# Optimization experiments

Hardware: AMD Instinct MI355X
Metric: run time of the kernel (lower is better)

Reference implementation:

```python
import jax, jax.numpy as jnp
import numpy as np

N, E, D = 100000, 1600000, 128      # nodes, edges, in_channels = MLP out_dim
L = 3                               # num GIN layers
OC = D + L * D                      # concat width = 512
CH, CHID = 4, 256                   # num ChannelMLPs, their hidden dim


def setup_inputs() -> dict:
    key = jax.random.key(0)
    ks = jax.random.split(key, 10)
    s = lambda fan_in: 1.0 / np.sqrt(fan_in)
    x = jax.random.normal(ks[0], (N, D), dtype=jnp.float32)
    edge_index = jax.random.randint(ks[1], (2, E), 0, N, dtype=jnp.int32)
    # conv MLPs: per layer 3 linear layers (in->hid, hid->hid, hid->out), all 128x128
    convW = jax.random.normal(ks[2], (L, 3, D, D), dtype=jnp.float32) * s(D)
    convB = jnp.zeros((L, 3, D), dtype=jnp.float32)
    # channel MLPs: 512 -> 256 -> 256 -> 1, ReLU after every layer (output_activation='relu')
    chanW1 = jax.random.normal(ks[3], (CH, OC, CHID), dtype=jnp.float32) * s(OC)
    chanB1 = jnp.zeros((CH, CHID), dtype=jnp.float32)
    chanW2 = jax.random.normal(ks[4], (CH, CHID, CHID), dtype=jnp.float32) * s(CHID)
    chanB2 = jnp.zeros((CH, CHID), dtype=jnp.float32)
    chanW3 = jax.random.normal(ks[5], (CH, CHID, 1), dtype=jnp.float32) * s(CHID)
    chanB3 = jnp.zeros((CH, 1), dtype=jnp.float32)
    return {"x": x, "edge_index": edge_index, "convW": convW, "convB": convB,
            "chanW1": chanW1, "chanB1": chanB1, "chanW2": chanW2, "chanB2": chanB2,
            "chanW3": chanW3, "chanB3": chanB3}


def reference(x, edge_index, convW, convB, chanW1, chanB1, chanW2, chanB2, chanW3, chanB3):
    src, dst = edge_index[0], edge_index[1]
    n = x.shape[0]
    feats = [x]                      # skip_first_features=False -> keep input
    h = x
    for l in range(L):
        # GINConv, eps=0: mlp((1+eps)*h + sum_{j in N(i)} h_j)
        agg = jax.ops.segment_sum(h[src], dst, num_segments=n)  # scatter-add at targets
        h = h + agg
        for k in range(3):           # MLP: Lin+ReLU x3 (2 hidden + relu output activation)
            h = jax.nn.relu(h @ convW[l, k] + convB[l, k])
        feats.append(h)
    xcat = jnp.concatenate(feats, axis=1)                       # [N, 512]
    # channel MLPs vectorized over the channel axis c
    h1 = jax.nn.relu(jnp.einsum('nd,cdh->cnh', xcat, chanW1) + chanB1[:, None, :])
    h2 = jax.nn.relu(jnp.einsum('cnh,chk->cnk', h1, chanW2) + chanB2[:, None, :])
    h3 = jax.nn.relu(jnp.einsum('cnh,cho->cno', h2, chanW3) + chanB3[:, None, :])
    return jnp.transpose(h3[..., 0])                            # [N, num_ChannelMLPs]
```

## Files before the change

### kernel.cpp

```cpp
#include <hip/hip_runtime.h>
#include <hip/hip_bf16.h>

#define D 128
#define NLAYER 3
#define NCH 4

typedef __attribute__((ext_vector_type(8))) short short8;
typedef __attribute__((ext_vector_type(4))) float f32x4;

__device__ __forceinline__ ushort f2bf(float f) {
    unsigned int u = __builtin_bit_cast(unsigned int, f);
    u += 0x7fffu + ((u >> 16) & 1u);
    return (ushort)(u >> 16);
}
__device__ __forceinline__ float bflo(unsigned int u) {
    return __builtin_bit_cast(float, u << 16);
}
__device__ __forceinline__ float bfhi(unsigned int u) {
    return __builtin_bit_cast(float, u & 0xffff0000u);
}

#define FILL_CHUNK 4096
__global__ __launch_bounds__(256) void hist_part_kernel(
    const int* __restrict__ dst, int* __restrict__ deg,
    int E, int nPer, int N)
{
    int cls = blockIdx.x & 7;
    int base = (blockIdx.x >> 3) * FILL_CHUNK;
    int lo = cls * nPer;
    int hi = lo + nPer; if (hi > N) hi = N;
    int end = base + FILL_CHUNK; if (end > E) end = E;
    for (int e = base + threadIdx.x; e < end; e += 256) {
        int d = dst[e];
        if (d >= lo && d < hi) atomicAdd(&deg[d], 1);
    }
}

__global__ __launch_bounds__(256) void blocksum_kernel(
    const int* __restrict__ deg, int* __restrict__ bsum, int n)
{
    int i = blockIdx.x * 256 + threadIdx.x;
    int v = (i < n) ? deg[i] : 0;
#pragma unroll
    for (int o = 1; o < 64; o <<= 1) v += __shfl_xor(v, o);
    __shared__ int s[4];
    if ((threadIdx.x & 63) == 0) s[threadIdx.x >> 6] = v;
    __syncthreads();
    if (threadIdx.x == 0) bsum[blockIdx.x] = s[0] + s[1] + s[2] + s[3];
}

__global__ __launch_bounds__(512) void scanblk_kernel(
    const int* __restrict__ bsum, int* __restrict__ boff, int nb,
    int* __restrict__ offs, int n, int E)
{
    __shared__ int sh[512];
    int t = threadIdx.x;
    sh[t] = (t < nb) ? bsum[t] : 0;
    __syncthreads();
    for (int d = 1; d < 512; d <<= 1) {
        int v = (t >= d) ? sh[t - d] : 0;
        __syncthreads();
        sh[t] += v;
        __syncthreads();
    }
    if (t < nb) boff[t] = (t == 0) ? 0 : sh[t - 1];
    if (t == 0) offs[n] = E;
}

__global__ __launch_bounds__(256) void blockscan_kernel(
    const int* __restrict__ deg, const int* __restrict__ boff,
    int* __restrict__ offs, int* __restrict__ cursor, int n)
{
    __shared__ int sh[256];
    int t = threadIdx.x;
    int i = blockIdx.x * 256 + t;
    int v = (i < n) ? deg[i] : 0;
    sh[t] = v;
    __syncthreads();
    for (int d = 1; d < 256; d <<= 1) {
        int u = (t >= d) ? sh[t - d] : 0;
        __syncthreads();
        sh[t] += u;
        __syncthreads();
    }
    if (i < n) {
        int ex = boff[blockIdx.x] + sh[t] - v;
        offs[i] = ex; cursor[i] = ex;
    }
}

__global__ __launch_bounds__(256) void fill_part_kernel(
    const int* __restrict__ src, const int* __restrict__ dst,
    int* __restrict__ cursor, int* __restrict__ csr,
    int E, int nPer, int N)
{
    int cls = blockIdx.x & 7;
    int base = (blockIdx.x >> 3) * FILL_CHUNK;
    int lo = cls * nPer;
    int hi = lo + nPer; if (hi > N) hi = N;
    int end = base + FILL_CHUNK; if (end > E) end = E;
    for (int e = base + threadIdx.x; e < end; e += 256) {
        int d = dst[e];
        int s = src[e];
        if (d >= lo && d < hi) {
            int p = atomicAdd(&cursor[d], 1);
            csr[p] = s;
        }
    }
}

__global__ __launch_bounds__(256) void cvtx_kernel(
    const float* __restrict__ x, ushort* __restrict__ xb, int total8)
{
    int i = blockIdx.x * 256 + threadIdx.x;
    if (i >= total8) return;
    const float* gp = x + (size_t)i * 8;
    float4 v0 = *(const float4*)gp;
    float4 v1 = *(const float4*)(gp + 4);
    short8 pk;
    pk[0] = (short)f2bf(v0.x); pk[1] = (short)f2bf(v0.y);
    pk[2] = (short)f2bf(v0.z); pk[3] = (short)f2bf(v0.w);
    pk[4] = (short)f2bf(v1.x); pk[5] = (short)f2bf(v1.y);
    pk[6] = (short)f2bf(v1.z); pk[7] = (short)f2bf(v1.w);
    *(short8*)(xb + (size_t)i * 8) = pk;
}

__global__ void cvtW_kernel(const float* __restrict__ W, ushort* __restrict__ Wt,
                            int K, int Ncols) {
    __shared__ float tile[32][33];
    int c = blockIdx.z;
    int k0 = blockIdx.x * 32, n0 = blockIdx.y * 32;
    const float* Wc = W + (size_t)c * K * Ncols;
    ushort* Wtc = Wt + (size_t)c * K * Ncols;
    int tx = threadIdx.x & 31, ty = threadIdx.x >> 5;
#pragma unroll
    for (int i = 0; i < 4; ++i) {
        int k = k0 + ty + i * 8;
        tile[ty + i * 8][tx] = Wc[(size_t)k * Ncols + n0 + tx];
    }
    __syncthreads();
#pragma unroll
    for (int i = 0; i < 4; ++i) {
        int n = n0 + ty + i * 8;
        Wtc[(size_t)n * K + k0 + tx] = f2bf(tile[tx][ty + i * 8]);
    }
}

__global__ __launch_bounds__(256) void agg_bf16(
    const ushort* __restrict__ h,
    const int* __restrict__ offs, const int* __restrict__ csr,
    ushort* __restrict__ outb, int n)
{
    int node = (blockIdx.x * 256 + threadIdx.x) >> 4;
    int l16 = threadIdx.x & 15;
    if (node >= n) return;
    uint4 u = *((const uint4*)(h + (size_t)node * 128) + l16);
    float a0 = bflo(u.x), a1 = bfhi(u.x);
    float a2 = bflo(u.y), a3 = bfhi(u.y);
    float a4 = bflo(u.z), a5 = bfhi(u.z);
    float a6 = bflo(u.w), a7 = bfhi(u.w);
    int b = offs[node], e = offs[node + 1];
    int j = b;
    for (; j + 4 <= e; j += 4) {
        int s0 = csr[j], s1 = csr[j + 1], s2 = csr[j + 2], s3 = csr[j + 3];
        uint4 v0 = *((const uint4*)(h + (size_t)s0 * 128) + l16);
        uint4 v1 = *((const uint4*)(h + (size_t)s1 * 128) + l16);
        uint4 v2 = *((const uint4*)(h + (size_t)s2 * 128) + l16);
        uint4 v3 = *((const uint4*)(h + (size_t)s3 * 128) + l16);
        a0 += (bflo(v0.x) + bflo(v1.x)) + (bflo(v2.x) + bflo(v3.x));
        a1 += (bfhi(v0.x) + bfhi(v1.x)) + (bfhi(v2.x) + bfhi(v3.x));
        a2 += (bflo(v0.y) + bflo(v1.y)) + (bflo(v2.y) + bflo(v3.y));
        a3 += (bfhi(v0.y) + bfhi(v1.y)) + (bfhi(v2.y) + bfhi(v3.y));
        a4 += (bflo(v0.z) + bflo(v1.z)) + (bflo(v2.z) + bflo(v3.z));
        a5 += (bfhi(v0.z) + bfhi(v1.z)) + (bfhi(v2.z) + bfhi(v3.z));
        a6 += (bflo(v0.w) + bflo(v1.w)) + (bflo(v2.w) + bflo(v3.w));
        a7 += (bfhi(v0.w) + bfhi(v1.w)) + (bfhi(v2.w) + bfhi(v3.w));
    }
    for (; j < e; ++j) {
        uint4 v0 = *((const uint4*)(h + (size_t)csr[j] * 128) + l16);
        a0 += bflo(v0.x); a1 += bfhi(v0.x);
        a2 += bflo(v0.y); a3 += bfhi(v0.y);
        a4 += bflo(v0.z); a5 += bfhi(v0.z);
        a6 += bflo(v0.w); a7 += bfhi(v0.w);
    }
    uint4 po;
    po.x = (unsigned int)f2bf(a0) | ((unsigned int)f2bf(a1) << 16);
    po.y = (unsigned int)f2bf(a2) | ((unsigned int)f2bf(a3) << 16);
    po.z = (unsigned int)f2bf(a4) | ((unsigned int)f2bf(a5) << 16);
    po.w = (unsigned int)f2bf(a6) | ((unsigned int)f2bf(a7) << 16);
    *((uint4*)(outb + (size_t)node * 128) + l16) = po;
}

__global__ __launch_bounds__(256) void gin_mlp_mfma(
    const ushort* __restrict__ A,
    const ushort* __restrict__ WtL,
    const float* __restrict__ biasL,
    ushort* __restrict__ Out,
    int nrows)
{
    __shared__ __align__(16) ushort As[128 * 128];
    __shared__ __align__(16) ushort Bs[128 * 128];
    const int t = threadIdx.x;
    const int w = t >> 6, lane = t & 63;
    const int quad = lane >> 4, c15 = lane & 15;
    const int wr = w >> 1, wc = w & 1;
    const int rowbase = blockIdx.x * 128;

#pragma unroll
    for (int i = 0; i < 8; ++i) {
        int lin = (i * 4 + w) * 64 + lane;
        int row = lin >> 4, slot = lin & 15, g = slot ^ (row & 15);
        int grow = rowbase + row;
        if (grow >= nrows) grow = 0;
        const ushort* gp = A + (size_t)grow * 128 + g * 8;
        __builtin_amdgcn_global_load_lds(
            (const __attribute__((address_space(1))) void*)gp,
            (__attribute__((address_space(3))) void*)&As[(i * 4 + w) * 512],
            16, 0, 0);
    }
#pragma unroll
    for (int i = 0; i < 8; ++i) {
        int lin = (i * 4 + w) * 64 + lane;
        int n = lin >> 4, slot = lin & 15, g = slot ^ (n & 15);
        const ushort* gp = WtL + (size_t)n * 128 + g * 8;
        __builtin_amdgcn_global_load_lds(
            (const __attribute__((address_space(1))) void*)gp,
            (__attribute__((address_space(3))) void*)&Bs[(i * 4 + w) * 512],
            16, 0, 0);
    }
    __syncthreads();

    for (int s = 0; s < 3; ++s) {
        f32x4 acc[4][4];
#pragma unroll
        for (int i = 0; i < 4; ++i)
#pragma unroll
            for (int j = 0; j < 4; ++j)
#pragma unroll
                for (int r = 0; r < 4; ++r) acc[i][j][r] = 0.f;

#pragma unroll
        for (int ks = 0; ks < 4; ++ks) {
            short8 af[4], bf[4];
#pragma unroll
            for (int tr = 0; tr < 4; ++tr) {
                int r = wr * 64 + tr * 16 + c15;
                af[tr] = *(const short8*)&As[r * 128 + (((ks * 4 + quad) ^ (r & 15)) * 8)];
            }
#pragma unroll
            for (int tc = 0; tc < 4; ++tc) {
                int n = wc * 64 + tc * 16 + c15;
                bf[tc] = *(const short8*)&Bs[n * 128 + (((ks * 4 + quad) ^ (n & 15)) * 8)];
            }
#pragma unroll
            for (int tr = 0; tr < 4; ++tr)
#pragma unroll
                for (int tc = 0; tc < 4; ++tc)
                    acc[tr][tc] = __builtin_amdgcn_mfma_f32_16x16x32_bf16(
                        af[tr], bf[tc], acc[tr][tc], 0, 0, 0);
        }
        __syncthreads();

        if (s < 2) {
#pragma unroll
            for (int tc = 0; tc < 4; ++tc) {
                int col = wc * 64 + tc * 16 + c15;
                float bv = biasL[s * 128 + col];
#pragma unroll
                for (int tr = 0; tr < 4; ++tr)
#pragma unroll
                    for (int rg = 0; rg < 4; ++rg) {
                        int row = wr * 64 + tr * 16 + quad * 4 + rg;
                        As[row * 128 + (((col >> 3) ^ (row & 15)) * 8) + (col & 7)]
                            = f2bf(fmaxf(acc[tr][tc][rg] + bv, 0.f));
                    }
            }
            const ushort* Wn = WtL + (size_t)(s + 1) * 128 * 128;
#pragma unroll
            for (int i = 0; i < 8; ++i) {
                int lin = (i * 4 + w) * 64 + lane;
                int n = lin >> 4, slot = lin & 15, g = slot ^ (n & 15);
                const ushort* gp = Wn + (size_t)n * 128 + g * 8;
                __builtin_amdgcn_global_load_lds(
                    (const __attribute__((address_space(1))) void*)gp,
                    (__attribute__((address_space(3))) void*)&Bs[(i * 4 + w) * 512],
                    16, 0, 0);
            }
            __syncthreads();
        } else {
#pragma unroll
            for (int tc = 0; tc < 4; ++tc) {
                int col = wc * 64 + tc * 16 + c15;
                float bv = biasL[2 * 128 + col];
#pragma unroll
                for (int tr = 0; tr < 4; ++tr)
#pragma unroll
                    for (int rg = 0; rg < 4; ++rg) {
                        int grow = rowbase + wr * 64 + tr * 16 + quad * 4 + rg;
                        if (grow < nrows)
                            Out[(size_t)grow * 128 + col]
                                = f2bf(fmaxf(acc[tr][tc][rg] + bv, 0.f));
                    }
            }
        }
    }
}

__global__ __launch_bounds__(256, 2) void chan_fused_mfma(
    const ushort* __restrict__ A0, const ushort* __restrict__ A1,
    const ushort* __restrict__ A2, const ushort* __restrict__ A3,
    const ushort* __restrict__ Wt1,
    const float* __restrict__ b1,
    const ushort* __restrict__ Wt2,
    const float* __restrict__ b2,
    const float* __restrict__ w3,
    const float* __restrict__ b3,
    float* __restrict__ out,
    int N, int T, int chunkT)
{
    const int bid = blockIdx.x;
    const int xcd = bid & 7;
    const int idx = bid >> 3;
    const int c = idx & 3;
    const int rt = xcd * chunkT + (idx >> 2);
    if (rt >= T) return;
    const int rowbase = rt * 64;

    __shared__ __align__(16) ushort As2[2][64 * 64];
    __shared__ __align__(16) ushort Bs2[2][256 * 64];
    ushort* Ts = &Bs2[1][0];
    float (*red)[4] = (float (*)[4]) & As2[0][0];

    const int t = threadIdx.x;
    const int w = t >> 6, lane = t & 63;
    const int quad = lane >> 4, c15 = lane & 15;
    const ushort* W1c = Wt1 + (size_t)c * 256 * 512;
    const ushort* W2c = Wt2 + (size_t)c * 256 * 256;

    int a_grow[2], a_g[2];
#pragma unroll
    for (int i = 0; i < 2; ++i) {
        int lin = (i * 4 + w) * 64 + lane;
        int row = lin >> 3, slot = lin & 7;
        a_g[i] = slot ^ (row & 7);
        int g = rowbase + row;
        a_grow[i] = (g < N) ? g : 0;
    }
    auto stageA = [&](int buf, int kc) {
        int ai = kc >> 7;
        const ushort* Ab = (ai == 0) ? A0 : (ai == 1) ? A1 : (ai == 2) ? A2 : A3;
        const int within = kc & 127;
#pragma unroll
        for (int i = 0; i < 2; ++i) {
            const ushort* gp = Ab + (size_t)a_grow[i] * 128 + within + a_g[i] * 8;
            __builtin_amdgcn_global_load_lds(
                (const __attribute__((address_space(1))) void*)gp,
                (__attribute__((address_space(3))) void*)&As2[buf][(i * 4 + w) * 512],
                16, 0, 0);
        }
    };
    int b_n[8], b_g[8];
#pragma unroll
    for (int i = 0; i < 8; ++i) {
        int lin = (i * 4 + w) * 64 + lane;
        b_n[i] = lin >> 3;
        b_g[i] = (lin & 7) ^ (b_n[i] & 7);
    }
    auto stageB = [&](int buf, const ushort* Wn, int ldk, int kc) {
#pragma unroll
        for (int i = 0; i < 8; ++i) {
            const ushort* gp = Wn + (size_t)b_n[i] * ldk + kc + b_g[i] * 8;
            __builtin_amdgcn_global_load_lds(
                (const __attribute__((address_space(1))) void*)gp,
                (__attribute__((address_space(3))) void*)&Bs2[buf][(i * 4 + w) * 512],
                16, 0, 0);
        }
    };

    f32x4 acc[4][4];
#pragma unroll
    for (int i = 0; i < 4; ++i)
#pragma unroll
        for (int j = 0; j < 4; ++j)
#pragma unroll
            for (int r = 0; r < 4; ++r) acc[i][j][r] = 0.f;

    stageA(1, 0);
    stageB(1, W1c, 512, 0);
#pragma unroll
    for (int s = 0; s < 8; ++s) {
        const int cur = (s + 1) & 1;
        if (s < 7) {
            stageA(cur ^ 1, (s + 1) * 64);
            stageB(cur ^ 1, W1c, 512, (s + 1) * 64);
            asm volatile("s_waitcnt vmcnt(10)" ::: "memory");
        } else {
            asm volatile("s_waitcnt vmcnt(0)" ::: "memory");
        }
        __builtin_amdgcn_s_barrier();
        __builtin_amdgcn_sched_barrier(0);
#pragma unroll
        for (int ks = 0; ks < 2; ++ks) {
            short8 af[4], bf[4];
#pragma unroll
            for (int tr = 0; tr < 4; ++tr) {
                int r = tr * 16 + c15;
                af[tr] = *(const short8*)&As2[cur][r * 64 + (((ks * 4 + quad) ^ (r & 7)) * 8)];
            }
#pragma unroll
            for (int tc = 0; tc < 4; ++tc) {
                int n = w * 64 + tc * 16 + c15;
                bf[tc] = *(const short8*)&Bs2[cur][n * 64 + (((ks * 4 + quad) ^ (n & 7)) * 8)];
            }
#pragma unroll
            for (int tr = 0; tr < 4; ++tr)
#pragma unroll
                for (int tc = 0; tc < 4; ++tc)
                    acc[tr][tc] = __builtin_amdgcn_mfma_f32_16x16x32_bf16(
                        af[tr], bf[tc], acc[tr][tc], 0, 0, 0);
        }
        __builtin_amdgcn_s_barrier();
    }

    stageB(0, W2c, 256, 0);
#pragma unroll
    for (int tc = 0; tc < 4; ++tc) {
        int col = w * 64 + tc * 16 + c15;
        float bv = b1[c * 256 + col];
#pragma unroll
        for (int tr = 0; tr < 4; ++tr)
#pragma unroll
            for (int rg = 0; rg < 4; ++rg) {
                int row = tr * 16 + quad * 4 + rg;
                Ts[row * 256 + (((col >> 3) ^ (row & 31)) * 8) + (col & 7)]
                    = f2bf(fmaxf(acc[tr][tc][rg] + bv, 0.f));
            }
    }
    __syncthreads();

#pragma unroll
    for (int i = 0; i < 4; ++i)
#pragma unroll
        for (int j = 0; j < 4; ++j)
#pragma unroll
            for (int r = 0; r < 4; ++r) acc[i][j][r] = 0.f;

#pragma unroll
    for (int s = 0; s < 4; ++s) {
#pragma unroll
        for (int ks = 0; ks < 2; ++ks) {
            short8 af[4], bf[4];
            const int g0 = s * 8 + ks * 4 + quad;
#pragma unroll
            for (int tr = 0; tr < 4; ++tr) {
                int r = tr * 16 + c15;
                af[tr] = *(const short8*)&Ts[r * 256 + ((g0 ^ (r & 31)) * 8)];
            }
#pragma unroll
            for (int tc = 0; tc < 4; ++tc) {
                int n = w * 64 + tc * 16 + c15;
                bf[tc] = *(const short8*)&Bs2[0][n * 64 + (((ks * 4 + quad) ^ (n & 7)) * 8)];
            }
#pragma unroll
            for (int tr = 0; tr < 4; ++tr)
#pragma unroll
                for (int tc = 0; tc < 4; ++tc)
                    acc[tr][tc] = __builtin_amdgcn_mfma_f32_16x16x32_bf16(
                        af[tr], bf[tc], acc[tr][tc], 0, 0, 0);
        }
        if (s < 3) {
            __syncthreads();
            stageB(0, W2c, 256, (s + 1) * 64);
            __syncthreads();
        }
    }

    float b2v[4], w3v[4];
#pragma unroll
    for (int tc = 0; tc < 4; ++tc) {
        int col = w * 64 + tc * 16 + c15;
        b2v[tc] = b2[c * 256 + col];
        w3v[tc] = w3[c * 256 + col];
    }
    __syncthreads();
#pragma unroll
    for (int tr = 0; tr < 4; ++tr)
#pragma unroll
        for (int rg = 0; rg < 4; ++rg) {
            float p = 0.f;
#pragma unroll
            for (int tc = 0; tc < 4; ++tc)
                p += fmaxf(acc[tr][tc][rg] + b2v[tc], 0.f) * w3v[tc];
            p += __shfl_xor(p, 1);
            p += __shfl_xor(p, 2);
            p += __shfl_xor(p, 4);
            p += __shfl_xor(p, 8);
            if (c15 == 0) red[tr * 16 + quad * 4 + rg][w] = p;
        }
    __syncthreads();
    if (t < 64) {
        int grow = rowbase + t;
        if (grow < N) {
            float s = red[t][0] + red[t][1] + red[t][2] + red[t][3] + b3[c];
            out[(size_t)grow * NCH + c] = fmaxf(s, 0.f);
        }
    }
}

extern "C" void kernel_launch(void* const* d_in, const int* in_sizes, int n_in,
                              void* d_out, int out_size, void* d_ws, size_t ws_size,
                              hipStream_t stream) {
    const float* x        = (const float*)d_in[0];
    const int*   eidx     = (const int*)d_in[1];
    const float* convW    = (const float*)d_in[2];
    const float* convB    = (const float*)d_in[3];
    const float* chanW1   = (const float*)d_in[4];
    const float* chanB1   = (const float*)d_in[5];
    const float* chanW2   = (const float*)d_in[6];
    const float* chanB2   = (const float*)d_in[7];
    const float* chanW3   = (const float*)d_in[8];
    const float* chanB3   = (const float*)d_in[9];
    float* out = (float*)d_out;

    const int N = in_sizes[0] / D;
    const int E = in_sizes[1] / 2;
    const int* srcp = eidx;
    const int* dstp = eidx + E;
    const int nb = (N + 255) / 256;

    char* w = (char*)d_ws;
    auto take = [&](size_t bytes) {
        char* p = w;
        w += (bytes + 255) & ~(size_t)255;
        return p;
    };
    ushort* xb     = (ushort*)take((size_t)N * D * 2);
    ushort* h0     = (ushort*)take((size_t)N * D * 2);
    ushort* h1     = (ushort*)take((size_t)N * D * 2);
    ushort* h2     = (ushort*)take((size_t)N * D * 2);
    int*    deg    = (int*)take((size_t)N * 4);
    int*    offs   = (int*)take((size_t)(N + 1) * 4);
    int*    cursor = (int*)take((size_t)N * 4);
    int*    bsum   = (int*)take((size_t)nb * 4);
    int*    boff   = (int*)take((size_t)nb * 4);
    ushort* Wt1b   = (ushort*)take((size_t)NCH * 256 * 512 * 2);
    ushort* Wt2b   = (ushort*)take((size_t)NCH * 256 * 256 * 2);
    ushort* WtC    = (ushort*)take((size_t)NLAYER * 3 * D * D * 2);

    size_t used = (size_t)(w - (char*)d_ws);
    if (used > ws_size) return;
    size_t rem = ws_size - used;
    size_t need_gin = (((size_t)E * 4 + 255) & ~(size_t)255) + (size_t)N * D * 2;
    if (rem < need_gin) return;

    int*    csr = (int*)w;
    ushort* a   = (ushort*)(w + (((size_t)E * 4 + 255) & ~(size_t)255));

    hipMemsetAsync(deg, 0, (size_t)N * 4, stream);
    {
        int nchunks = (E + FILL_CHUNK - 1) / FILL_CHUNK;
        int nPer = (N + 7) / 8;
        hist_part_kernel<<<nchunks * 8, 256, 0, stream>>>(dstp, deg, E, nPer, N);
        blocksum_kernel<<<nb, 256, 0, stream>>>(deg, bsum, N);
        scanblk_kernel<<<1, 512, 0, stream>>>(bsum, boff, nb, offs, N, E);
        blockscan_kernel<<<nb, 256, 0, stream>>>(deg, boff, offs, cursor, N);
        fill_part_kernel<<<nchunks * 8, 256, 0, stream>>>(
            srcp, dstp, cursor, csr, E, nPer, N);
    }

    cvtx_kernel<<<(N * 16 + 255) / 256, 256, 0, stream>>>(x, xb, N * 16);
    cvtW_kernel<<<dim3(512 / 32, 256 / 32, NCH), 256, 0, stream>>>(chanW1, Wt1b, 512, 256);
    cvtW_kernel<<<dim3(256 / 32, 256 / 32, NCH), 256, 0, stream>>>(chanW2, Wt2b, 256, 256);
    cvtW_kernel<<<dim3(D / 32, D / 32, NLAYER * 3), 256, 0, stream>>>(convW, WtC, D, D);

    const int rowtiles = (N + 127) / 128;
    const int aggblocks = (N * 16 + 255) / 256;

    ushort* hbuf[NLAYER] = {h0, h1, h2};
    const ushort* prev = xb;
    for (int l = 0; l < NLAYER; ++l) {
        agg_bf16<<<aggblocks, 256, 0, stream>>>(prev, offs, csr, a, N);
        gin_mlp_mfma<<<rowtiles, 256, 0, stream>>>(
            a, WtC + (size_t)l * 3 * D * D, convB + (size_t)l * 3 * D, hbuf[l], N);
        prev = hbuf[l];
    }

    {
        const int T = (N + 63) / 64;
        const int chunkT = (T + 7) / 8;
        const int grid = 8 * chunkT * NCH;
        chan_fused_mfma<<<grid, 256, 0, stream>>>(
            xb, h0, h1, h2,
            Wt1b, chanB1, Wt2b, chanB2, chanW3, chanB3,
            out, N, T, chunkT);
    }
}
```

Measured before the change: 822.2 us.

## Load channel-MLP weight fragments directly into registers instead of LDS staging

The B-operand (weights) of both GEMMs in the fused channel MLP is now read straight from global memory into MFMA register fragments, with register double-buffering in the first GEMM. The LDS staging buffers for B are removed, so LDS use drops from about 80KB to about 48KB, and launch bounds are raised to allow 3 blocks per CU. This also removes the per-step barriers in the second GEMM. The trade-off is uncoalesced, partly exposed global/L2 loads of weights per wave, along with higher register pressure under the tighter occupancy bound.

```diff
diff --git a/kernel.cpp b/kernel.cpp
--- a/kernel.cpp
+++ b/kernel.cpp
@@ -306,7 +306,7 @@
     }
 }
 
-__global__ __launch_bounds__(256, 2) void chan_fused_mfma(
+__global__ __launch_bounds__(256, 3) void chan_fused_mfma(
     const ushort* __restrict__ A0, const ushort* __restrict__ A1,
     const ushort* __restrict__ A2, const ushort* __restrict__ A3,
     const ushort* __restrict__ Wt1,
@@ -327,8 +327,7 @@
     const int rowbase = rt * 64;
 
     __shared__ __align__(16) ushort As2[2][64 * 64];
-    __shared__ __align__(16) ushort Bs2[2][256 * 64];
-    ushort* Ts = &Bs2[1][0];
+    __shared__ __align__(16) ushort Ts[64 * 256];
     float (*red)[4] = (float (*)[4]) & As2[0][0];
 
     const int t = threadIdx.x;
@@ -359,22 +358,15 @@
                 16, 0, 0);
         }
     };
-    int b_n[8], b_g[8];
-#pragma unroll
-    for (int i = 0; i < 8; ++i) {
-        int lin = (i * 4 + w) * 64 + lane;
-        b_n[i] = lin >> 3;
-        b_g[i] = (lin & 7) ^ (b_n[i] & 7);
-    }
-    auto stageB = [&](int buf, const ushort* Wn, int ldk, int kc) {
-#pragma unroll
-        for (int i = 0; i < 8; ++i) {
-            const ushort* gp = Wn + (size_t)b_n[i] * ldk + kc + b_g[i] * 8;
-            __builtin_amdgcn_global_load_lds(
-                (const __attribute__((address_space(1))) void*)gp,
-                (__attribute__((address_space(3))) void*)&Bs2[buf][(i * 4 + w) * 512],
-                16, 0, 0);
-        }
+
+    int ncol[4];
+#pragma unroll
+    for (int tc = 0; tc < 4; ++tc) ncol[tc] = w * 64 + tc * 16 + c15;
+
+    auto loadB = [&](short8 (&dst)[4], const ushort* Wn, int ldk, int kc, int ks) {
+#pragma unroll
+        for (int tc = 0; tc < 4; ++tc)
+            dst[tc] = *(const short8*)&Wn[(size_t)ncol[tc] * ldk + kc + (ks * 4 + quad) * 8];
     };
 
     f32x4 acc[4][4];
@@ -385,47 +377,58 @@
 #pragma unroll
             for (int r = 0; r < 4; ++r) acc[i][j][r] = 0.f;
 
+    short8 bfb[2][4];
+    loadB(bfb[0], W1c, 512, 0, 0);
     stageA(1, 0);
-    stageB(1, W1c, 512, 0);
 #pragma unroll
     for (int s = 0; s < 8; ++s) {
         const int cur = (s + 1) & 1;
+        const int bb = s & 1;
+        short8 bf1[4];
+        loadB(bf1, W1c, 512, s * 64, 1);
         if (s < 7) {
+            loadB(bfb[bb ^ 1], W1c, 512, (s + 1) * 64, 0);
             stageA(cur ^ 1, (s + 1) * 64);
-            stageB(cur ^ 1, W1c, 512, (s + 1) * 64);
             asm volatile("s_waitcnt vmcnt(10)" ::: "memory");
         } else {
-            asm volatile("s_waitcnt vmcnt(0)" ::: "memory");
+            asm volatile("s_waitcnt vmcnt(4)" ::: "memory");
         }
         __builtin_amdgcn_s_barrier();
         __builtin_amdgcn_sched_barrier(0);
-#pragma unroll
-        for (int ks = 0; ks < 2; ++ks) {
-            short8 af[4], bf[4];
+        {
+            short8 af[4];
 #pragma unroll
             for (int tr = 0; tr < 4; ++tr) {
                 int r = tr * 16 + c15;
-                af[tr] = *(const short8*)&As2[cur][r * 64 + (((ks * 4 + quad) ^ (r & 7)) * 8)];
-            }
-#pragma unroll
-            for (int tc = 0; tc < 4; ++tc) {
-                int n = w * 64 + tc * 16 + c15;
-                bf[tc] = *(const short8*)&Bs2[cur][n * 64 + (((ks * 4 + quad) ^ (n & 7)) * 8)];
+                af[tr] = *(const short8*)&As2[cur][r * 64 + ((quad ^ (r & 7)) * 8)];
             }
 #pragma unroll
             for (int tr = 0; tr < 4; ++tr)
 #pragma unroll
                 for (int tc = 0; tc < 4; ++tc)
                     acc[tr][tc] = __builtin_amdgcn_mfma_f32_16x16x32_bf16(
-                        af[tr], bf[tc], acc[tr][tc], 0, 0, 0);
+                        af[tr], bfb[bb][tc], acc[tr][tc], 0, 0, 0);
+        }
+        {
+            short8 af[4];
+#pragma unroll
+            for (int tr = 0; tr < 4; ++tr) {
+                int r = tr * 16 + c15;
+                af[tr] = *(const short8*)&As2[cur][r * 64 + (((4 + quad) ^ (r & 7)) * 8)];
+            }
+#pragma unroll
+            for (int tr = 0; tr < 4; ++tr)
+#pragma unroll
+                for (int tc = 0; tc < 4; ++tc)
+                    acc[tr][tc] = __builtin_amdgcn_mfma_f32_16x16x32_bf16(
+                        af[tr], bf1[tc], acc[tr][tc], 0, 0, 0);
         }
         __builtin_amdgcn_s_barrier();
     }
 
-    stageB(0, W2c, 256, 0);
 #pragma unroll
     for (int tc = 0; tc < 4; ++tc) {
-        int col = w * 64 + tc * 16 + c15;
+        int col = ncol[tc];
         float bv = b1[c * 256 + col];
 #pragma unroll
         for (int tr = 0; tr < 4; ++tr)
@@ -451,34 +454,25 @@
         for (int ks = 0; ks < 2; ++ks) {
             short8 af[4], bf[4];
             const int g0 = s * 8 + ks * 4 + quad;
+            loadB(bf, W2c, 256, s * 64, ks);
 #pragma unroll
             for (int tr = 0; tr < 4; ++tr) {
                 int r = tr * 16 + c15;
                 af[tr] = *(const short8*)&Ts[r * 256 + ((g0 ^ (r & 31)) * 8)];
             }
 #pragma unroll
-            for (int tc = 0; tc < 4; ++tc) {
-                int n = w * 64 + tc * 16 + c15;
-                bf[tc] = *(const short8*)&Bs2[0][n * 64 + (((ks * 4 + quad) ^ (n & 7)) * 8)];
-            }
-#pragma unroll
             for (int tr = 0; tr < 4; ++tr)
 #pragma unroll
                 for (int tc = 0; tc < 4; ++tc)
                     acc[tr][tc] = __builtin_amdgcn_mfma_f32_16x16x32_bf16(
                         af[tr], bf[tc], acc[tr][tc], 0, 0, 0);
         }
-        if (s < 3) {
-            __syncthreads();
-            stageB(0, W2c, 256, (s + 1) * 64);
-            __syncthreads();
-        }
     }
 
     float b2v[4], w3v[4];
 #pragma unroll
     for (int tc = 0; tc < 4; ++tc) {
-        int col = w * 64 + tc * 16 + c15;
+        int col = ncol[tc];
         b2v[tc] = b2[c * 256 + col];
         w3v[tc] = w3[c * 256 + col];
     }
```

After: 920.9 us. +12.0%, slower.
